# Optimization experiments

Hardware: AMD Instinct MI355X
Metric: run time of the kernel (lower is better)

## Reference

```python
import jax, jax.numpy as jnp
import numpy as np

NEG = -1e30

def setup_inputs() -> dict:
    key = jax.random.key(0)
    k1, k2, k3, k4, k5, k6, k7, k8 = jax.random.split(key, 8)
    B, Ti, Tm = 4, 512, 1024
    Din, Dmem, D = 256, 256, 64
    inputs = jax.random.normal(k1, (B, Ti, Din), dtype=jnp.float32)
    memory = jax.random.normal(k2, (B, Tm, Dmem), dtype=jnp.float32)
    input_lengths = jax.random.randint(k3, (B,), 1, Ti + 1)
    memory_lengths = jax.random.randint(k4, (B,), 1, Tm + 1)
    s_in = 1.0 / np.sqrt(Din)
    s_d = 1.0 / np.sqrt(D)
    W_in = jax.random.uniform(k5, (D, Din), jnp.float32, -s_in, s_in)
    b_in = jax.random.uniform(k6, (D,), jnp.float32, -s_in, s_in)
    W_mem = jax.random.uniform(k7, (D, Dmem), jnp.float32, -s_in, s_in)
    W_final = jax.random.uniform(k8, (D,), jnp.float32, -s_d, s_d)
    return {"inputs": inputs, "memory": memory,
            "input_lengths": input_lengths, "memory_lengths": memory_lengths,
            "W_in": W_in, "b_in": b_in, "W_mem": W_mem, "W_final": W_final}

def reference(inputs, memory, input_lengths, memory_lengths, W_in, b_in, W_mem, W_final):
    # inputs: (B,Ti,Din), memory: (B,Tm,Dmem)
    input_item = jnp.einsum('bid,td->bit', inputs, W_in) + b_in      # (B,Ti,D)
    memory_item = jnp.einsum('bmd,td->bmt', memory, W_mem)           # (B,Tm,D)
    items = jnp.tanh(input_item[:, :, None, :] + memory_item[:, None, :, :])  # (B,Ti,Tm,D)
    score = jnp.einsum('bitd,d->bit'.replace('t', 'mt')[:0] or 'bimd,d->bim', items, W_final)  # (B,Ti,Tm)
    Ti = inputs.shape[-2]
    Tm = memory.shape[-2]
    in_mask = jnp.arange(Ti)[None, :] < input_lengths[:, None]       # (B,Ti)
    mem_mask = jnp.arange(Tm)[None, :] < memory_lengths[:, None]     # (B,Tm)
    score = jnp.where(in_mask[:, :, None], score, NEG)
    score = jnp.where(mem_mask[:, None, :], score, NEG)
    attn = jax.nn.softmax(score, axis=-1)                            # (B,Ti,Tm)
    out = jnp.einsum('bim,bmd->bid', attn, memory)                   # (B,Ti,Dmem)
    return out
```

## Files before the change

kernel.cpp:

```cpp
#include <hip/hip_runtime.h>

#define C2  2.8853900817779268f
#define L2E 1.4426950408889634f

__global__ __launch_bounds__(256) void proj_kernel(
    const float* __restrict__ inputs, const float* __restrict__ memory,
    const float* __restrict__ W_in, const float* __restrict__ b_in,
    const float* __restrict__ W_mem,
    float* __restrict__ in_item, float* __restrict__ mem_item)
{
  const int NIN = 2048;
  int r0 = blockIdx.x * 16;
  int tid = threadIdx.x;
  __shared__ float4 wlds[64][64];

  const float* Wsel; const float* Abase; float* O; int ar0; bool has_bias = (r0 < NIN);
  if (has_bias) { Wsel = W_in;  Abase = inputs; O = in_item;  ar0 = r0; }
  else          { Wsel = W_mem; Abase = memory; O = mem_item; ar0 = r0 - NIN; }

  const float4* Wv = reinterpret_cast<const float4*>(Wsel);
  #pragma unroll
  for (int u = 0; u < 16; ++u) {
    int e = tid + u * 256;
    int k4 = e & 63, dd = e >> 6;
    wlds[k4][dd ^ (k4 & 7)] = Wv[e];
  }
  int d = tid & 63, rg = tid >> 6;
  float bias = has_bias ? b_in[d] : 0.f;
  __syncthreads();

  const float4* A0 = reinterpret_cast<const float4*>(Abase + (size_t)(ar0 + rg) * 256);
  float acc0 = 0.f, acc1 = 0.f, acc2 = 0.f, acc3 = 0.f;
  #pragma unroll 8
  for (int k4 = 0; k4 < 64; ++k4) {
    float4 w  = wlds[k4][d ^ (k4 & 7)];
    float4 a0 = A0[k4];
    float4 a1 = A0[k4 + 256];
    float4 a2 = A0[k4 + 512];
    float4 a3 = A0[k4 + 768];
    acc0 += a0.x*w.x + a0.y*w.y + a0.z*w.z + a0.w*w.w;
    acc1 += a1.x*w.x + a1.y*w.y + a1.z*w.z + a1.w*w.w;
    acc2 += a2.x*w.x + a2.y*w.y + a2.z*w.z + a2.w*w.w;
    acc3 += a3.x*w.x + a3.y*w.y + a3.z*w.z + a3.w*w.w;
  }
  O[(size_t)(ar0 + rg     ) * 64 + d] = (acc0 + bias) * C2;
  O[(size_t)(ar0 + rg +  4) * 64 + d] = (acc1 + bias) * C2;
  O[(size_t)(ar0 + rg +  8) * 64 + d] = (acc2 + bias) * C2;
  O[(size_t)(ar0 + rg + 12) * 64 + d] = (acc3 + bias) * C2;
}

__global__ __launch_bounds__(512, 4) void attn_kernel(
    const float* __restrict__ in_item,
    const float* __restrict__ mem_item,
    const float* __restrict__ memory,
    const int* __restrict__ in_len, const int* __restrict__ mem_len,
    const float* __restrict__ W_final,
    float* __restrict__ out)
{
  const int Ti = 512, Tm = 1024, DM = 256;
  const int TI = 4, MT = 128, NT = 8;
  int b = blockIdx.y;
  int i0 = blockIdx.x * TI;
  int tid = threadIdx.x;

  __shared__ float4 smem[16 * 128];
  __shared__ float4 pt4[128];
  __shared__ float  red[8];

  const int s_ii = __builtin_amdgcn_readfirstlane(tid >> 7);
  const int s_ml = tid & 127;
  const int dq = tid & 63, wv_ = tid >> 6;

  float4 qreg[16];
  {
    const float4* qrow = reinterpret_cast<const float4*>(
        in_item + ((size_t)b * Ti + i0 + s_ii) * 64);
    #pragma unroll
    for (int j = 0; j < 16; ++j) qreg[j] = qrow[j];
  }

  float Wsum = 0.f;
  #pragma unroll
  for (int j = 0; j < 64; ++j) Wsum += W_final[j];
  const float c1 = L2E * Wsum;
  const float4* Wf4 = reinterpret_cast<const float4*>(W_final);

  int ilen = in_len[b], mlen = mem_len[b];
  const bool row_valid = (i0 + s_ii) < ilen;

  const float4* mem4 = reinterpret_cast<const float4*>(mem_item);
  const float* memb = memory + (size_t)b * Tm * DM;

  float psum = 0.f;
  float4 a0 = make_float4(0,0,0,0), a1 = a0, a2 = a0, a3 = a0;

  #pragma unroll
  for (int u = 0; u < 4; ++u) {
    int e = tid + u * 512, dd4 = e & 15, mm = e >> 4;
    smem[dd4 * 128 + (mm ^ (dd4 & 7))] = mem4[((size_t)b * Tm + mm) * 16 + dd4];
  }
  __syncthreads();

  #pragma unroll 1
  for (int t = 0; t < NT; ++t) {
    int m0 = t * MT;

    float4 S4 = make_float4(0,0,0,0);
    #pragma unroll
    for (int d4 = 0; d4 < 16; ++d4) {
      float4 mv = smem[d4 * 128 + (s_ml ^ (d4 & 7))];
      float4 qv = qreg[d4];
      float4 w  = Wf4[d4];
      S4.x = fmaf(w.x, __builtin_amdgcn_rcpf(1.0f + __builtin_amdgcn_exp2f(qv.x + mv.x)), S4.x);
      S4.y = fmaf(w.y, __builtin_amdgcn_rcpf(1.0f + __builtin_amdgcn_exp2f(qv.y + mv.y)), S4.y);
      S4.z = fmaf(w.z, __builtin_amdgcn_rcpf(1.0f + __builtin_amdgcn_exp2f(qv.z + mv.z)), S4.z);
      S4.w = fmaf(w.w, __builtin_amdgcn_rcpf(1.0f + __builtin_amdgcn_exp2f(qv.w + mv.w)), S4.w);
    }
    float S = (S4.x + S4.y) + (S4.z + S4.w);
    int m = m0 + s_ml;
    float p = row_valid ? ((m < mlen) ? __builtin_amdgcn_exp2f(fmaf(-C2, S, c1)) : 0.f)
                        : 1.0f;
    reinterpret_cast<float*>(&pt4[s_ml])[s_ii] = p;
    psum += p;
    __syncthreads();

    if (t + 1 < NT) {
      int m0n = m0 + MT;
      #pragma unroll
      for (int u = 0; u < 4; ++u) {
        int e = tid + u * 512, dd4 = e & 15, mm = e >> 4;
        smem[dd4 * 128 + (mm ^ (dd4 & 7))] = mem4[((size_t)b * Tm + m0n + mm) * 16 + dd4];
      }
    }

    {
      const float* mpb = memb + (size_t)(m0 + wv_ * 16) * DM + dq * 4;
      #pragma unroll
      for (int mm = 0; mm < 16; ++mm) {
        float4 v = *reinterpret_cast<const float4*>(mpb + (size_t)mm * DM);
        float4 pp = pt4[wv_ * 16 + mm];
        a0.x += pp.x*v.x; a0.y += pp.x*v.y; a0.z += pp.x*v.z; a0.w += pp.x*v.w;
        a1.x += pp.y*v.x; a1.y += pp.y*v.y; a1.z += pp.y*v.z; a1.w += pp.y*v.w;
        a2.x += pp.z*v.x; a2.y += pp.z*v.y; a2.z += pp.z*v.z; a2.w += pp.z*v.w;
        a3.x += pp.w*v.x; a3.y += pp.w*v.y; a3.z += pp.w*v.z; a3.w += pp.w*v.w;
      }
    }
    __syncthreads();
  }

  {
    float s = psum;
    #pragma unroll
    for (int o = 32; o >= 1; o >>= 1) s += __shfl_xor(s, o);
    if (dq == 0) red[wv_] = s;
  }
  smem[(wv_ * 4 + 0) * 64 + dq] = a0;
  smem[(wv_ * 4 + 1) * 64 + dq] = a1;
  smem[(wv_ * 4 + 2) * 64 + dq] = a2;
  smem[(wv_ * 4 + 3) * 64 + dq] = a3;
  __syncthreads();

  if (tid < 256) {
    int ii = tid >> 6, d2 = tid & 63;
    float4 s = smem[ii * 64 + d2];
    #pragma unroll
    for (int w = 1; w < 8; ++w) {
      float4 v = smem[(w * 4 + ii) * 64 + d2];
      s.x += v.x; s.y += v.y; s.z += v.z; s.w += v.w;
    }
    float inv = __builtin_amdgcn_rcpf(red[2 * ii] + red[2 * ii + 1]);
    s.x *= inv; s.y *= inv; s.z *= inv; s.w *= inv;
    reinterpret_cast<float4*>(out)[((size_t)b * Ti + i0 + ii) * 64 + d2] = s;
  }
}

extern "C" void kernel_launch(void* const* d_in, const int* in_sizes, int n_in,
                              void* d_out, int out_size, void* d_ws, size_t ws_size,
                              hipStream_t stream) {
  const float* inputs   = (const float*)d_in[0];
  const float* memory   = (const float*)d_in[1];
  const int*   in_len   = (const int*)  d_in[2];
  const int*   mem_len  = (const int*)  d_in[3];
  const float* W_in     = (const float*)d_in[4];
  const float* b_in     = (const float*)d_in[5];
  const float* W_mem    = (const float*)d_in[6];
  const float* W_final  = (const float*)d_in[7];
  float* out = (float*)d_out;

  float* in_item  = (float*)d_ws;
  float* mem_item = in_item + 2048 * 64;

  proj_kernel<<<384, 256, 0, stream>>>(inputs, memory, W_in, b_in, W_mem,
                                       in_item, mem_item);
  attn_kernel<<<dim3(128, 4), 512, 0, stream>>>(in_item, mem_item, memory,
                                                in_len, mem_len, W_final, out);
}
```

Measured before the change: 74.41 us.

## Split attention over memory dimension into two partial blocks plus combine kernel

Splits the Tm loop of the attention kernel across a new grid z dimension, so each block handles half of memory and writes an unnormalized partial output and partial probability sum to workspace. A new combine kernel sums the partials and normalizes. This doubles the block count (512 to 1024) to improve occupancy and latency hiding on the many CUs. In exchange it adds an extra launch and extra global traffic for the partial buffers, and it depends on sufficient workspace size. The fixed exponent offset (no running max) makes the split safe.

```diff
diff --git a/kernel.cpp b/kernel.cpp
--- a/kernel.cpp
+++ b/kernel.cpp
@@ -55,12 +55,17 @@
     const float* __restrict__ memory,
     const int* __restrict__ in_len, const int* __restrict__ mem_len,
     const float* __restrict__ W_final,
-    float* __restrict__ out)
+    float* __restrict__ o_part,
+    float* __restrict__ psum_part,
+    int m_count)
 {
   const int Ti = 512, Tm = 1024, DM = 256;
-  const int TI = 4, MT = 128, NT = 8;
+  const int TI = 4, MT = 128;
+  const int NT = m_count >> 7;
   int b = blockIdx.y;
   int i0 = blockIdx.x * TI;
+  int z = blockIdx.z;
+  int m_begin = z * m_count;
   int tid = threadIdx.x;
 
   __shared__ float4 smem[16 * 128];
@@ -97,13 +102,13 @@
   #pragma unroll
   for (int u = 0; u < 4; ++u) {
     int e = tid + u * 512, dd4 = e & 15, mm = e >> 4;
-    smem[dd4 * 128 + (mm ^ (dd4 & 7))] = mem4[((size_t)b * Tm + mm) * 16 + dd4];
+    smem[dd4 * 128 + (mm ^ (dd4 & 7))] = mem4[((size_t)b * Tm + m_begin + mm) * 16 + dd4];
   }
   __syncthreads();
 
   #pragma unroll 1
   for (int t = 0; t < NT; ++t) {
-    int m0 = t * MT;
+    int m0 = m_begin + t * MT;
 
     float4 S4 = make_float4(0,0,0,0);
     #pragma unroll
@@ -168,10 +173,31 @@
       float4 v = smem[(w * 4 + ii) * 64 + d2];
       s.x += v.x; s.y += v.y; s.z += v.z; s.w += v.w;
     }
-    float inv = __builtin_amdgcn_rcpf(red[2 * ii] + red[2 * ii + 1]);
-    s.x *= inv; s.y *= inv; s.z *= inv; s.w *= inv;
-    reinterpret_cast<float4*>(out)[((size_t)b * Ti + i0 + ii) * 64 + d2] = s;
-  }
+    size_t r = (size_t)b * Ti + i0 + ii;
+    reinterpret_cast<float4*>(o_part)[((size_t)z * 2048 + r) * 64 + d2] = s;
+  }
+  if (tid < TI) {
+    psum_part[(size_t)z * 2048 + (size_t)b * Ti + i0 + tid] = red[2 * tid] + red[2 * tid + 1];
+  }
+}
+
+__global__ __launch_bounds__(256) void combine_kernel(
+    const float* __restrict__ o_part, const float* __restrict__ psum_part,
+    float* __restrict__ out, int nsplit)
+{
+  int e = blockIdx.x * 256 + threadIdx.x;
+  int r = e >> 6;
+  const float4* op4 = reinterpret_cast<const float4*>(o_part);
+  float4 o = op4[e];
+  float s = psum_part[r];
+  if (nsplit == 2) {
+    float4 o1 = op4[e + 131072];
+    o.x += o1.x; o.y += o1.y; o.z += o1.z; o.w += o1.w;
+    s += psum_part[r + 2048];
+  }
+  float inv = __builtin_amdgcn_rcpf(s);
+  o.x *= inv; o.y *= inv; o.z *= inv; o.w *= inv;
+  reinterpret_cast<float4*>(out)[e] = o;
 }
 
 extern "C" void kernel_launch(void* const* d_in, const int* in_sizes, int n_in,
@@ -187,11 +213,18 @@
   const float* W_final  = (const float*)d_in[7];
   float* out = (float*)d_out;
 
-  float* in_item  = (float*)d_ws;
-  float* mem_item = in_item + 2048 * 64;
+  float* in_item   = (float*)d_ws;
+  float* mem_item  = in_item + 2048 * 64;
+  float* o_part    = mem_item + 4096 * 64;
+  float* psum_part = o_part + 2 * 2048 * 256;
+
+  size_t need2 = (size_t)(131072 + 262144 + 2 * 524288 + 2 * 2048 + 64) * 4;
+  int nsplit = (ws_size >= need2) ? 2 : 1;
 
   proj_kernel<<<384, 256, 0, stream>>>(inputs, memory, W_in, b_in, W_mem,
                                        in_item, mem_item);
-  attn_kernel<<<dim3(128, 4), 512, 0, stream>>>(in_item, mem_item, memory,
-                                                in_len, mem_len, W_final, out);
-}
+  attn_kernel<<<dim3(128, 4, nsplit), 512, 0, stream>>>(
+      in_item, mem_item, memory, in_len, mem_len, W_final,
+      o_part, psum_part, 1024 / nsplit);
+  combine_kernel<<<512, 256, 0, stream>>>(o_part, psum_part, out, nsplit);
+}
```

New measurement: 79.42 us. +6.7%, slower.
